# Performance work log

Measured on AMD Instinct MI355X. Metric: run time of the kernel, lower is better.

Reference implementation:

```python
import jax, jax.numpy as jnp
import numpy as np

EMBED_DIM = 1024
NUM_HEADS = 16
HEAD_DIM = EMBED_DIM // NUM_HEADS


def setup_inputs() -> dict:
    key = jax.random.key(0)
    ks = jax.random.split(key, 6)
    s = 1.0 / np.sqrt(EMBED_DIM)
    return {
        "x": jax.random.normal(ks[0], (4, 2048, EMBED_DIM), dtype=jnp.float32),
        "Wq": jax.random.uniform(ks[1], (EMBED_DIM, EMBED_DIM), jnp.float32, -s, s),
        "Wk": jax.random.uniform(ks[2], (EMBED_DIM, EMBED_DIM), jnp.float32, -s, s),
        "Wv": jax.random.uniform(ks[3], (EMBED_DIM, EMBED_DIM), jnp.float32, -s, s),
        "Wo": jax.random.uniform(ks[4], (EMBED_DIM, EMBED_DIM), jnp.float32, -s, s),
        "bo": jax.random.uniform(ks[5], (EMBED_DIM,), jnp.float32, -s, s),
    }


def reference(x, Wq, Wk, Wv, Wo, bo):
    B, S, E = x.shape
    H, D = NUM_HEADS, HEAD_DIM
    # torch Linear: x @ W.T ; reshape to [B, H, S, D]
    q = (x @ Wq.T).reshape(B, S, H, D).transpose(0, 2, 1, 3)
    k = (x @ Wk.T).reshape(B, S, H, D).transpose(0, 2, 1, 3)
    v = (x @ Wv.T).reshape(B, S, H, D).transpose(0, 2, 1, 3)
    scores = jnp.einsum("bhqd,bhkd->bhqk", q, k) / jnp.sqrt(jnp.float32(D))
    attn = jax.nn.softmax(scores, axis=-1)  # dropout is identity in eval mode
    out = jnp.einsum("bhqk,bhkd->bhqd", attn, v)
    out = out.transpose(0, 2, 1, 3).reshape(B, S, E)
    return out @ Wo.T + bo
```

## Files before the change

kernel.cpp:

```cpp
#include <hip/hip_runtime.h>
#include <hip/hip_bf16.h>
#include <math.h>

#define B_ 4
#define S_ 2048
#define E_ 1024
#define H_ 16
#define D_ 64
#define M_ (B_*S_)
#define NKV 32

typedef __attribute__((ext_vector_type(8))) short short8;
typedef __attribute__((ext_vector_type(4))) short short4_t;
typedef __attribute__((ext_vector_type(4))) float f32x4;
typedef __attribute__((ext_vector_type(16))) float f32x16;

static __device__ __forceinline__ short f2bf(float f){
  union { float f; unsigned u; } v; v.f = f;
  unsigned u = v.u + 0x7FFFu + ((v.u >> 16) & 1u);
  return (short)(u >> 16);
}

__global__ void cast_all(const float* __restrict__ x,
    const float* __restrict__ wq, const float* __restrict__ wk,
    const float* __restrict__ wv, const float* __restrict__ wo,
    short8* __restrict__ xb, short8* __restrict__ wqb, short8* __restrict__ wkb,
    short8* __restrict__ wvb, short8* __restrict__ wob){
  int bid = blockIdx.x;
  const float* src; short8* dst; int i;
  if (bid < 4096) { src = x; dst = xb; i = bid*256 + threadIdx.x; }
  else {
    int k = (bid - 4096) >> 9;
    i = ((bid - 4096) & 511)*256 + threadIdx.x;
    src = k==0 ? wq : k==1 ? wk : k==2 ? wv : wo;
    dst = k==0 ? wqb : k==1 ? wkb : k==2 ? wvb : wob;
  }
  const float4* s4 = (const float4*)src;
  float4 a = s4[2*i], b = s4[2*i+1];
  short8 o;
  o[0]=f2bf(a.x); o[1]=f2bf(a.y); o[2]=f2bf(a.z); o[3]=f2bf(a.w);
  o[4]=f2bf(b.x); o[5]=f2bf(b.y); o[6]=f2bf(b.z); o[7]=f2bf(b.w);
  dst[i]=o;
}

#define GLOAD16(g, l) __builtin_amdgcn_global_load_lds( \
    (const __attribute__((address_space(1))) void*)(g), \
    (__attribute__((address_space(3))) void*)(l), 16, 0, 0)

__global__ __launch_bounds__(256,2) void gemm_qkv(const short* __restrict__ A,
      const short* __restrict__ Wf, short* __restrict__ Qo, short* __restrict__ Ko,
      short* __restrict__ Vto, float u)
{
  __shared__ short AL[128*32];
  __shared__ short BL[128*32];
  const int tid = threadIdx.x;
  const int w = tid >> 6, lane = tid & 63;
  const int l15 = lane & 15, l4 = lane >> 4;
  const int m0 = blockIdx.x * 128;
  const int n0 = blockIdx.y * 128;
  const int wr = w >> 1, wc = w & 1;
  f32x4 acc[4][4] = {};

  const short* ga = A  + (size_t)(m0 + (tid>>2))*1024 + (tid&3)*8;
  const short* gb = Wf + (size_t)(n0 + (tid>>2))*1024 + (tid&3)*8;

  for (int kt = 0; kt < 32; ++kt) {
    const int ko = kt*32;
    #pragma unroll
    for (int p = 0; p < 2; ++p) {
      GLOAD16(ga + (size_t)(p*64)*1024 + ko, (char*)AL + p*4096 + w*1024);
      GLOAD16(gb + (size_t)(p*64)*1024 + ko, (char*)BL + p*4096 + w*1024);
    }
    __syncthreads();
    short8 af[4], bw[4];
    #pragma unroll
    for (int i = 0; i < 4; ++i) {
      af[i] = *(const short8*)(AL + (wr*64 + i*16 + l15)*32 + 8*l4);
      bw[i] = *(const short8*)(BL + (wc*64 + i*16 + l15)*32 + 8*l4);
    }
    #pragma unroll
    for (int i = 0; i < 4; ++i)
      #pragma unroll
      for (int j = 0; j < 4; ++j)
        acc[i][j] = __builtin_amdgcn_mfma_f32_16x16x32_bf16(af[i], bw[j], acc[i][j], 0,0,0);
    __syncthreads();
  }

  const int sel = n0 >> 10;
  const int nc0 = n0 & 1023;
  if (sel == 2) {
    #pragma unroll
    for (int i = 0; i < 4; ++i) {
      int row = m0 + wr*64 + i*16 + 4*l4;
      int b = row >> 11;
      int s0 = row & 2047;
      #pragma unroll
      for (int j = 0; j < 4; ++j) {
        int col = nc0 + wc*64 + j*16 + l15;
        int h = col >> 6, d = col & 63;
        short4_t pk;
        pk[0]=f2bf(acc[i][j][0]); pk[1]=f2bf(acc[i][j][1]);
        pk[2]=f2bf(acc[i][j][2]); pk[3]=f2bf(acc[i][j][3]);
        *(short4_t*)(Vto + (((size_t)(b*H_ + h))*D_ + d)*S_ + s0) = pk;
      }
    }
  } else {
    short* O = sel ? Ko : Qo;
    float sc = sel ? 1.0f : u;
    #pragma unroll
    for (int i = 0; i < 4; ++i) {
      int row = m0 + wr*64 + i*16 + 4*l4;
      int b = row >> 11;
      #pragma unroll
      for (int j = 0; j < 4; ++j) {
        int col = nc0 + wc*64 + j*16 + l15;
        int h = col >> 6, d = col & 63;
        #pragma unroll
        for (int r = 0; r < 4; ++r) {
          int s = (row + r) & 2047;
          O[(((size_t)(b*H_ + h))*S_ + s)*D_ + d] = f2bf(acc[i][j][r]*sc);
        }
      }
    }
  }
}

__global__ __launch_bounds__(256,2) void gemm_out(const short* __restrict__ A,
      const short* __restrict__ W, float* __restrict__ out,
      const float* __restrict__ bias)
{
  __shared__ short AL[128*32];
  __shared__ short BL[128*32];
  const int tid = threadIdx.x;
  const int w = tid >> 6, lane = tid & 63;
  const int l15 = lane & 15, l4 = lane >> 4;
  const int m0 = blockIdx.x * 128;
  const int n0 = blockIdx.y * 128;
  const int wr = w >> 1, wc = w & 1;
  f32x4 acc[4][4] = {};

  const short* ga = A + (size_t)(m0 + (tid>>2))*1024 + (tid&3)*8;
  const short* gb = W + (size_t)(n0 + (tid>>2))*1024 + (tid&3)*8;

  for (int kt = 0; kt < 32; ++kt) {
    const int ko = kt*32;
    #pragma unroll
    for (int p = 0; p < 2; ++p) {
      GLOAD16(ga + (size_t)(p*64)*1024 + ko, (char*)AL + p*4096 + w*1024);
      GLOAD16(gb + (size_t)(p*64)*1024 + ko, (char*)BL + p*4096 + w*1024);
    }
    __syncthreads();
    short8 af[4], bw[4];
    #pragma unroll
    for (int i = 0; i < 4; ++i) {
      af[i] = *(const short8*)(AL + (wr*64 + i*16 + l15)*32 + 8*l4);
      bw[i] = *(const short8*)(BL + (wc*64 + i*16 + l15)*32 + 8*l4);
    }
    #pragma unroll
    for (int i = 0; i < 4; ++i)
      #pragma unroll
      for (int j = 0; j < 4; ++j)
        acc[i][j] = __builtin_amdgcn_mfma_f32_16x16x32_bf16(af[i], bw[j], acc[i][j], 0,0,0);
    __syncthreads();
  }

  #pragma unroll
  for (int i = 0; i < 4; ++i) {
    int row = m0 + wr*64 + i*16 + 4*l4;
    #pragma unroll
    for (int j = 0; j < 4; ++j) {
      int col = n0 + wc*64 + j*16 + l15;
      float bz = bias[col];
      #pragma unroll
      for (int r = 0; r < 4; ++r)
        out[(size_t)(row + r)*1024 + col] = acc[i][j][r] + bz;
    }
  }
}

static __device__ __forceinline__ unsigned cvtpk(float lo, float hi){
  unsigned d; asm("v_cvt_pk_bf16_f32 %0, %1, %2" : "=v"(d) : "v"(lo), "v"(hi)); return d;
}
static __device__ __forceinline__ void plswap(unsigned &a, unsigned &b){
  asm("v_permlane32_swap_b32 %0, %1" : "+v"(a), "+v"(b));
}
template<int BASE>
static __device__ __forceinline__ short8 pfrag(const f32x16 &s){
  unsigned w01 = cvtpk(s[BASE+0], s[BASE+1]);
  unsigned w23 = cvtpk(s[BASE+2], s[BASE+3]);
  unsigned w45 = cvtpk(s[BASE+4], s[BASE+5]);
  unsigned w67 = cvtpk(s[BASE+6], s[BASE+7]);
  plswap(w01, w45);
  plswap(w23, w67);
  union { unsigned u[4]; short8 s8; } r;
  r.u[0]=w01; r.u[1]=w23; r.u[2]=w45; r.u[3]=w67;
  return r.s8;
}

__global__ __launch_bounds__(256,4) void attn_kernel(const short* __restrict__ Qb,
    const short* __restrict__ Kb, const short* __restrict__ Vtb, short* __restrict__ Ob)
{
  __shared__ short KL[2][64*64];
  __shared__ short VL[2][64*64];
  const int tid = threadIdx.x, w = tid >> 6, lane = tid & 63;
  const int l31 = lane & 31, hi = lane >> 5;
  const int rx7 = l31 & 7;

  const int linear = blockIdx.x;
  const int swz = (linear & 7)*128 + (linear >> 3);
  const int bh = swz >> 4;
  const int b = bh >> 4, h = bh & 15;
  const int q0 = (swz & 15) * 128;

  const short* Qg = Qb + ((size_t)bh*S_ + q0)*D_;
  const short* Kg = Kb + (size_t)bh*S_*D_;
  const short* Vg = Vtb + (size_t)bh*D_*S_;

  const int srow = tid >> 3;
  const int scol = ((tid & 7) ^ (srow & 7)) * 8;

  #define STAGE(t, bi) { \
    GLOAD16(Kg + (size_t)((t)*64 +      srow)*D_ + scol, (char*)KL[bi] + w*1024); \
    GLOAD16(Kg + (size_t)((t)*64 + 32 + srow)*D_ + scol, (char*)KL[bi] + 4096 + w*1024); \
    GLOAD16(Vg + (size_t)(     srow)*S_ + (t)*64 + scol, (char*)VL[bi] + w*1024); \
    GLOAD16(Vg + (size_t)(32 + srow)*S_ + (t)*64 + scol, (char*)VL[bi] + 4096 + w*1024); }

  STAGE(0, 0)

  const int qrow = w*32 + l31;
  short8 qf[4];
  #pragma unroll
  for (int t = 0; t < 4; ++t)
    qf[t] = *(const short8*)(Qg + (size_t)qrow*D_ + (2*t + hi)*8);

  f32x16 oacc[2] = {};
  float l_run = 0.f;

  for (int kv = 0; kv < NKV; ++kv) {
    const int cur = kv & 1;
    if (kv < NKV-1) {
      STAGE(kv+1, cur^1)
      asm volatile("s_waitcnt vmcnt(4)" ::: "memory");
    } else {
      asm volatile("s_waitcnt vmcnt(0)" ::: "memory");
    }
    __builtin_amdgcn_s_barrier();
    asm volatile("" ::: "memory");
    __builtin_amdgcn_sched_barrier(0);

    f32x16 st[2] = {};
    __builtin_amdgcn_s_setprio(1);
    #pragma unroll
    for (int t = 0; t < 4; ++t) {
      int co = ((2*t + hi) ^ rx7)*16;
      short8 ka0 = *(const short8*)((char*)KL[cur] + l31*128 + co);
      short8 ka1 = *(const short8*)((char*)KL[cur] + (32 + l31)*128 + co);
      st[0] = __builtin_amdgcn_mfma_f32_32x32x16_bf16(ka0, qf[t], st[0], 0,0,0);
      st[1] = __builtin_amdgcn_mfma_f32_32x32x16_bf16(ka1, qf[t], st[1], 0,0,0);
    }
    __builtin_amdgcn_s_setprio(0);

    #pragma unroll
    for (int r = 0; r < 16; ++r) st[0][r] = __builtin_amdgcn_exp2f(st[0][r]);
    #pragma unroll
    for (int r = 0; r < 16; ++r) st[1][r] = __builtin_amdgcn_exp2f(st[1][r]);
    {
      f32x16 sv = st[0] + st[1];
      float sa = (sv[0]+sv[1]) + (sv[2]+sv[3]);
      float sb = (sv[4]+sv[5]) + (sv[6]+sv[7]);
      float sc = (sv[8]+sv[9]) + (sv[10]+sv[11]);
      float sd = (sv[12]+sv[13]) + (sv[14]+sv[15]);
      l_run += (sa+sb) + (sc+sd);
    }

    short8 pf[4];
    pf[0] = pfrag<0>(st[0]);
    pf[1] = pfrag<8>(st[0]);
    pf[2] = pfrag<0>(st[1]);
    pf[3] = pfrag<8>(st[1]);

    __builtin_amdgcn_s_setprio(1);
    #pragma unroll
    for (int t = 0; t < 4; ++t) {
      int co = ((2*t + hi) ^ rx7)*16;
      short8 va0 = *(const short8*)((char*)VL[cur] + l31*128 + co);
      short8 va1 = *(const short8*)((char*)VL[cur] + (32 + l31)*128 + co);
      oacc[0] = __builtin_amdgcn_mfma_f32_32x32x16_bf16(va0, pf[t], oacc[0], 0,0,0);
      oacc[1] = __builtin_amdgcn_mfma_f32_32x32x16_bf16(va1, pf[t], oacc[1], 0,0,0);
    }
    __builtin_amdgcn_s_setprio(0);
    __builtin_amdgcn_sched_barrier(0);
    asm volatile("" ::: "memory");
    __builtin_amdgcn_s_barrier();
    asm volatile("" ::: "memory");
  }
  #undef STAGE

  float lt = l_run + __shfl_xor(l_run, 32);
  float inv = 1.f / lt;
  int s = q0 + qrow;
  short* orow = Ob + ((size_t)(b*S_ + s))*E_ + h*64;
  #pragma unroll
  for (int r = 0; r < 16; r += 2) {
    int d0 = (r & 3) + 8*(r >> 2) + 4*hi;
    unsigned pa = (unsigned short)f2bf(oacc[0][r]*inv) |
                  ((unsigned)(unsigned short)f2bf(oacc[0][r+1]*inv) << 16);
    unsigned pb = (unsigned short)f2bf(oacc[1][r]*inv) |
                  ((unsigned)(unsigned short)f2bf(oacc[1][r+1]*inv) << 16);
    *(unsigned*)(orow + d0) = pa;
    *(unsigned*)(orow + 32 + d0) = pb;
  }
}

extern "C" void kernel_launch(void* const* d_in, const int* in_sizes, int n_in,
                              void* d_out, int out_size, void* d_ws, size_t ws_size,
                              hipStream_t stream) {
  const float* x  = (const float*)d_in[0];
  const float* Wq = (const float*)d_in[1];
  const float* Wk = (const float*)d_in[2];
  const float* Wv = (const float*)d_in[3];
  const float* Wo = (const float*)d_in[4];
  const float* bo = (const float*)d_in[5];

  char* ws = (char*)d_ws;
  short* xb  = (short*)(ws);
  short* Wqb = (short*)(ws + (16u<<20));
  short* Wkb = (short*)(ws + (18u<<20));
  short* Wvb = (short*)(ws + (20u<<20));
  short* Wob = (short*)(ws + (22u<<20));
  short* Qb  = (short*)(ws + (24u<<20));
  short* Kb  = (short*)(ws + (40u<<20));
  short* Vtb = (short*)(ws + (56u<<20));
  short* Ab  = (short*)(ws + (72u<<20));

  cast_all<<<4096 + 4*512, 256, 0, stream>>>(x, Wq, Wk, Wv, Wo,
      (short8*)xb, (short8*)Wqb, (short8*)Wkb, (short8*)Wvb, (short8*)Wob);

  const float u = 0.18033688011112042f;
  gemm_qkv<<<dim3(64, 24), 256, 0, stream>>>(xb, Wqb, Qb, Kb, Vtb, u);

  attn_kernel<<<1024, 256, 0, stream>>>(Qb, Kb, Vtb, Ab);

  gemm_out<<<dim3(64, 8), 256, 0, stream>>>(Ab, Wob, (float*)d_out, bo);
}
```

Baseline: 188.9 us.

## Rewrite QKV GEMM as 256x256 tile, double-buffered LDS, 8-wave interleaved pipeline

The QKV projection GEMM moves from 128x128 tiles with 4 waves and a single LDS buffer to 256x256 tiles with 8 waves and 128KB of double-buffered dynamic LDS. K steps are 64 wide, and the loads for the next step are interleaved with MFMA quadrants under explicit barriers and priority hints. The LDS chunk index is XOR-swizzled to avoid bank conflicts. Together these aim to hide global load latency and raise data reuse, at the cost of higher register and LDS pressure (occupancy is probably limited to one block per CU) and a smaller grid of 384 blocks.

```diff
diff --git a/kernel.cpp b/kernel.cpp
--- a/kernel.cpp
+++ b/kernel.cpp
@@ -47,56 +47,99 @@
     (const __attribute__((address_space(1))) void*)(g), \
     (__attribute__((address_space(3))) void*)(l), 16, 0, 0)
 
-__global__ __launch_bounds__(256,2) void gemm_qkv(const short* __restrict__ A,
+__global__ __launch_bounds__(512,2) void gemm_qkv(const short* __restrict__ A,
       const short* __restrict__ Wf, short* __restrict__ Qo, short* __restrict__ Ko,
       short* __restrict__ Vto, float u)
 {
-  __shared__ short AL[128*32];
-  __shared__ short BL[128*32];
+  extern __shared__ char LDSc[];
   const int tid = threadIdx.x;
   const int w = tid >> 6, lane = tid & 63;
   const int l15 = lane & 15, l4 = lane >> 4;
-  const int m0 = blockIdx.x * 128;
-  const int n0 = blockIdx.y * 128;
-  const int wr = w >> 1, wc = w & 1;
-  f32x4 acc[4][4] = {};
-
-  const short* ga = A  + (size_t)(m0 + (tid>>2))*1024 + (tid&3)*8;
-  const short* gb = Wf + (size_t)(n0 + (tid>>2))*1024 + (tid&3)*8;
-
-  for (int kt = 0; kt < 32; ++kt) {
-    const int ko = kt*32;
-    #pragma unroll
-    for (int p = 0; p < 2; ++p) {
-      GLOAD16(ga + (size_t)(p*64)*1024 + ko, (char*)AL + p*4096 + w*1024);
-      GLOAD16(gb + (size_t)(p*64)*1024 + ko, (char*)BL + p*4096 + w*1024);
-    }
-    __syncthreads();
-    short8 af[4], bw[4];
-    #pragma unroll
-    for (int i = 0; i < 4; ++i) {
-      af[i] = *(const short8*)(AL + (wr*64 + i*16 + l15)*32 + 8*l4);
-      bw[i] = *(const short8*)(BL + (wc*64 + i*16 + l15)*32 + 8*l4);
-    }
-    #pragma unroll
-    for (int i = 0; i < 4; ++i)
-      #pragma unroll
-      for (int j = 0; j < 4; ++j)
-        acc[i][j] = __builtin_amdgcn_mfma_f32_16x16x32_bf16(af[i], bw[j], acc[i][j], 0,0,0);
-    __syncthreads();
-  }
+  const int rx = l15 & 7;
+  const int wm = w >> 2, wn = w & 3;
+  const int m0 = blockIdx.x * 256;
+  const int n0 = blockIdx.y * 256;
+
+  const int lanerow = lane >> 3;
+  const int lchunk8 = ((lane & 7) ^ lanerow) * 8;
+  const short* Aq = A  + (size_t)(m0 + w*8 + lanerow)*1024 + lchunk8;
+  const short* Bq = Wf + (size_t)(n0 + w*8 + lanerow)*1024 + lchunk8;
+
+  #define STA(kt,h,i) GLOAD16(Aq + (size_t)((h)*128 + (i)*64)*1024 + (kt)*64, \
+      LDSc + ((kt)&1)*65536 + (h)*16384 + (i)*8192 + w*1024);
+  #define STB(kt,h,i) GLOAD16(Bq + (size_t)((h)*128 + (i)*64)*1024 + (kt)*64, \
+      LDSc + ((kt)&1)*65536 + 32768 + (h)*16384 + (i)*8192 + w*1024);
+
+  #define BARF __builtin_amdgcn_s_barrier(); \
+               asm volatile("" ::: "memory"); \
+               __builtin_amdgcn_sched_barrier(0);
+
+  f32x4 acc[8][4] = {};
+
+  STA(0,0,0) STA(0,0,1) STA(0,1,0) STA(0,1,1)
+  STB(0,0,0) STB(0,0,1) STB(0,1,0) STB(0,1,1)
+  asm volatile("s_waitcnt vmcnt(0)" ::: "memory");
+  BARF
+
+  #define RDA(QM) \
+    _Pragma("unroll") for (int i_ = 0; i_ < 4; ++i_) \
+    _Pragma("unroll") for (int ks_ = 0; ks_ < 2; ++ks_) \
+      af_[i_][ks_] = *(const short8*)(Ab + (wm*128 + (QM)*64 + i_*16 + l15)*128 + (((ks_*4 + l4) ^ rx)*16));
+  #define RDB(DST,QN) \
+    _Pragma("unroll") for (int j_ = 0; j_ < 2; ++j_) \
+    _Pragma("unroll") for (int ks_ = 0; ks_ < 2; ++ks_) \
+      DST[j_][ks_] = *(const short8*)(Bb + (wn*64 + (QN)*32 + j_*16 + l15)*128 + (((ks_*4 + l4) ^ rx)*16));
+  #define MF(QM,QN,BF) \
+    __builtin_amdgcn_s_setprio(1); \
+    _Pragma("unroll") for (int i_ = 0; i_ < 4; ++i_) \
+    _Pragma("unroll") for (int j_ = 0; j_ < 2; ++j_) \
+    _Pragma("unroll") for (int ks_ = 0; ks_ < 2; ++ks_) \
+      acc[(QM)*4+i_][(QN)*2+j_] = __builtin_amdgcn_mfma_f32_16x16x32_bf16( \
+          af_[i_][ks_], BF[j_][ks_], acc[(QM)*4+i_][(QN)*2+j_], 0,0,0); \
+    __builtin_amdgcn_s_setprio(0);
+
+  for (int k = 0; k < 16; ++k) {
+    const char* Ab = LDSc + (k & 1)*65536;
+    const char* Bb = Ab + 32768;
+    const bool st = (k < 15);
+    short8 af_[4][2], b0_[2][2], b1_[2][2];
+    RDA(0)
+    RDB(b0_, 0)
+    if (st) { STA(k+1,0,0) STA(k+1,0,1) STA(k+1,1,0) STA(k+1,1,1) }
+    BARF
+    MF(0,0,b0_)
+    BARF
+    RDB(b1_, 1)
+    if (st) { STB(k+1,0,0) STB(k+1,0,1) }
+    BARF
+    MF(0,1,b1_)
+    BARF
+    RDA(1)
+    if (st) { STB(k+1,1,0) STB(k+1,1,1) }
+    BARF
+    MF(1,1,b1_)
+    BARF
+    MF(1,0,b0_)
+    asm volatile("s_waitcnt vmcnt(0)" ::: "memory");
+    BARF
+  }
+  #undef RDA
+  #undef RDB
+  #undef MF
+  #undef STA
+  #undef STB
 
   const int sel = n0 >> 10;
-  const int nc0 = n0 & 1023;
+  const int ncb = (n0 & 1023) + wn*64;
   if (sel == 2) {
     #pragma unroll
-    for (int i = 0; i < 4; ++i) {
-      int row = m0 + wr*64 + i*16 + 4*l4;
+    for (int i = 0; i < 8; ++i) {
+      int row = m0 + wm*128 + i*16 + 4*l4;
       int b = row >> 11;
       int s0 = row & 2047;
       #pragma unroll
       for (int j = 0; j < 4; ++j) {
-        int col = nc0 + wc*64 + j*16 + l15;
+        int col = ncb + j*16 + l15;
         int h = col >> 6, d = col & 63;
         short4_t pk;
         pk[0]=f2bf(acc[i][j][0]); pk[1]=f2bf(acc[i][j][1]);
@@ -108,12 +151,12 @@
     short* O = sel ? Ko : Qo;
     float sc = sel ? 1.0f : u;
     #pragma unroll
-    for (int i = 0; i < 4; ++i) {
-      int row = m0 + wr*64 + i*16 + 4*l4;
+    for (int i = 0; i < 8; ++i) {
+      int row = m0 + wm*128 + i*16 + 4*l4;
       int b = row >> 11;
       #pragma unroll
       for (int j = 0; j < 4; ++j) {
-        int col = nc0 + wc*64 + j*16 + l15;
+        int col = ncb + j*16 + l15;
         int h = col >> 6, d = col & 63;
         #pragma unroll
         for (int r = 0; r < 4; ++r) {
@@ -123,6 +166,7 @@
       }
     }
   }
+  #undef BARF
 }
 
 __global__ __launch_bounds__(256,2) void gemm_out(const short* __restrict__ A,
@@ -337,7 +381,7 @@
       (short8*)xb, (short8*)Wqb, (short8*)Wkb, (short8*)Wvb, (short8*)Wob);
 
   const float u = 0.18033688011112042f;
-  gemm_qkv<<<dim3(64, 24), 256, 0, stream>>>(xb, Wqb, Qb, Kb, Vtb, u);
+  gemm_qkv<<<dim3(32, 12), 512, 131072, stream>>>(xb, Wqb, Qb, Kb, Vtb, u);
 
   attn_kernel<<<1024, 256, 0, stream>>>(Qb, Kb, Vtb, Ab);
 
```

Result: no change. 185.6 us (-1.8%).
